# Performance work log

Hardware: AMD Instinct MI355X
Metric: run time of the kernel (lower is better)

## Reference

```python
import jax, jax.numpy as jnp
import numpy as np

B, C, H, W = 4, 3, 128, 128
HID = 128          # hidden_features
L = 6              # hidden_layers
NP = 5             # n_params
DT = 0.1
EPS = 1e-5         # PyG InstanceNorm eps
D_EMB = 1 + 2 + NP             # u + pos(2) + params
D_MSG = 2 * HID + 1 + 2 + NP   # x_i,x_j,u_i-u_j,pos_i-pos_j,vars_i
D_UPD = HID + HID + NP         # x, message, vars


def _build_edges(b, h, w):
    # 8-neighbor grid graph (radius_graph with r=sqrt(2), loop=False),
    # node index = ix*h + iy (x-major, matching create_graph's meshgrid flatten)
    ix, iy = np.meshgrid(np.arange(w), np.arange(h), indexing='ij')
    node = ix * h + iy
    srcs, tgts = [], []
    for dx in (-1, 0, 1):
        for dy in (-1, 0, 1):
            if dx == 0 and dy == 0:
                continue
            t = node[max(0, -dx):w - max(0, dx), max(0, -dy):h - max(0, dy)]
            s = node[max(0, dx):w - max(0, -dx), max(0, dy):h - max(0, -dy)]
            srcs.append(s.ravel()); tgts.append(t.ravel())
    src = np.concatenate(srcs); tgt = np.concatenate(tgts)
    offs = (np.arange(b) * h * w)[:, None]
    src = (src[None, :] + offs).ravel()
    tgt = (tgt[None, :] + offs).ravel()
    return np.stack([src, tgt]).astype(np.int32)


def _lin(key, fan_in, fan_out):
    kw, kb = jax.random.split(key)
    s = 1.0 / np.sqrt(fan_in)
    return (jax.random.uniform(kw, (fan_in, fan_out), jnp.float32, -s, s),
            jax.random.uniform(kb, (fan_out,), jnp.float32, -s, s))


def setup_inputs() -> dict:
    key = jax.random.key(0)
    ks = jax.random.split(key, 32)
    inputs = jax.random.normal(ks[0], (B, C, H, W), jnp.float32)
    case_params = jax.random.uniform(ks[1], (B, NP), jnp.float32, 0.5, 1.5)
    edge_index = jnp.asarray(_build_edges(B, H, W))

    emb_W1, emb_b1 = _lin(ks[2], D_EMB, HID)
    emb_W2, emb_b2 = _lin(ks[3], HID, HID)

    def stack(kbase, fan_in, fan_out):
        Ws, bs = [], []
        for l in range(L):
            Wl, bl = _lin(jax.random.fold_in(kbase, l), fan_in, fan_out)
            Ws.append(Wl); bs.append(bl)
        return jnp.stack(Ws), jnp.stack(bs)

    msg1_W, msg1_b = stack(ks[4], D_MSG, HID)
    msg2_W, msg2_b = stack(ks[5], HID, HID)
    upd1_W, upd1_b = stack(ks[6], D_UPD, HID)
    upd2_W, upd2_b = stack(ks[7], HID, HID)
    out_W1, out_b1 = _lin(ks[8], HID, HID // 2)
    out_W2, out_b2 = _lin(ks[9], HID // 2, 1)

    return dict(inputs=inputs, case_params=case_params, edge_index=edge_index,
                emb_W1=emb_W1, emb_b1=emb_b1, emb_W2=emb_W2, emb_b2=emb_b2,
                msg1_W=msg1_W, msg1_b=msg1_b, msg2_W=msg2_W, msg2_b=msg2_b,
                upd1_W=upd1_W, upd1_b=upd1_b, upd2_W=upd2_W, upd2_b=upd2_b,
                out_W1=out_W1, out_b1=out_b1, out_W2=out_W2, out_b2=out_b2)


def reference(inputs, case_params, edge_index,
              emb_W1, emb_b1, emb_W2, emb_b2,
              msg1_W, msg1_b, msg2_W, msg2_b,
              upd1_W, upd1_b, upd2_W, upd2_b,
              out_W1, out_b1, out_W2, out_b2):
    b, c, h, w = inputs.shape
    n = b * h * w
    swish = lambda x: x * jax.nn.sigmoid(x)

    # graph node features: [b,c,h,w] -> [b*h*w, c]; u = channel 0
    x_nodes = inputs.transpose(0, 2, 3, 1).reshape(-1, c)
    u = x_nodes[:, :1]
    # pos, faithful to create_graph: per-graph meshgrid over (x:w, y:h), x-major flatten
    gx = jnp.linspace(0., 1., w)[:, None] * jnp.ones((h,), inputs.dtype)   # [w,h]
    gy = jnp.ones((w,), inputs.dtype)[:, None] * jnp.linspace(0., 1., h)  # [w,h]
    pos = jnp.stack([gx[None] * case_params[:, 1, None, None],
                     gy[None] * case_params[:, 0, None, None]], axis=-1).reshape(-1, 2)
    params = jnp.repeat(case_params, h * w, axis=0)  # [n, NP]

    src, tgt = edge_index[0], edge_index[1]
    deg = jax.ops.segment_sum(jnp.ones_like(src, dtype=inputs.dtype), tgt,
                              num_segments=n)
    deg = jnp.maximum(deg, 1.)[:, None]

    # embedding MLP
    f = swish(jnp.concatenate([u, pos, params], -1) @ emb_W1 + emb_b1)
    f = swish(f @ emb_W2 + emb_b2)

    for l in range(msg1_W.shape[0]):
        # message: gather -> MLP (formula 8)
        m = jnp.concatenate([f[tgt], f[src], u[tgt] - u[src],
                             pos[tgt] - pos[src], params[tgt]], -1)  # [E, D_MSG]
        m = swish(m @ msg1_W[l] + msg1_b[l])
        m = swish(m @ msg2_W[l] + msg2_b[l])
        # mean-aggregate at target nodes
        agg = jax.ops.segment_sum(m, tgt, num_segments=n) / deg
        # update MLP (formula 9) + residual (in_features == out_features)
        upd = swish(jnp.concatenate([f, agg, params], -1) @ upd1_W[l] + upd1_b[l])
        upd = swish(upd @ upd2_W[l] + upd2_b[l])
        f = f + upd
        # InstanceNorm per graph (affine=False, biased var)
        fg = f.reshape(b, h * w, -1)
        mean = fg.mean(1, keepdims=True)
        var = ((fg - mean) ** 2).mean(1, keepdims=True)
        f = ((fg - mean) * jax.lax.rsqrt(var + EPS)).reshape(n, -1)

    diff = swish(f @ out_W1 + out_b1) @ out_W2 + out_b2  # [n,1]
    out = u + DT * diff
    return out.reshape(b, h, w, 1).transpose(0, 3, 1, 2)  # preds [b,1,h,w]
```

## Files before the change

### kernel.cpp

```cpp
#include <hip/hip_runtime.h>
#include <hip/hip_bf16.h>
#include <math.h>

#define NNODE 65536
#define NBAT  16384
#define NP    5
#define DT    0.1f
#define EPS   1e-5f

typedef __attribute__((ext_vector_type(8))) short short8;
typedef __attribute__((ext_vector_type(4))) float floatx4;

union S8U { short8 s; unsigned int u[4]; };

__device__ __forceinline__ float swishf(float x) {
    return x * __builtin_amdgcn_rcpf(1.f + __expf(-x));
}
__device__ __forceinline__ float asf(unsigned int u) {
    union { unsigned int u; float f; } x; x.u = u; return x.f;
}
__device__ __forceinline__ unsigned short f2b(float f) {
    union { float f; unsigned int u; } x; x.f = f;
    unsigned int r = x.u + 0x7fff + ((x.u >> 16) & 1);
    return (unsigned short)(r >> 16);
}
__device__ __forceinline__ unsigned int pk2(float a, float b) {
    __hip_bfloat162 h = __float22bfloat162_rn(make_float2(a, b));
    union { __hip_bfloat162 h; unsigned int u; } x; x.h = h; return x.u;
}

#define CHP(w, g, r15) ((((w) * 272) + (g) * 17 + (r15)) * 8)

__global__ __launch_bounds__(256) void prep_all(
    const float* __restrict__ msg1_W, const float* __restrict__ msg2_W,
    const float* __restrict__ upd1_W, const float* __restrict__ upd2_W,
    const float* __restrict__ emb_W2, const float* __restrict__ out_W1,
    unsigned short* __restrict__ wPT, unsigned short* __restrict__ wQT,
    unsigned short* __restrict__ w2F, unsigned short* __restrict__ u1aF,
    unsigned short* __restrict__ u1bF, unsigned short* __restrict__ u2F,
    unsigned short* __restrict__ eW2F, unsigned short* __restrict__ O1F)
{
    int blk = blockIdx.x;
    const float* src; unsigned short* dst;
    int ldn = 128, koff, NT = 8, lstride, perm = 1, i0;
    if (blk < 384)       { src = msg1_W; dst = wPT;  koff = 0;   lstride = 264 * 128; i0 = blk; }
    else if (blk < 768)  { src = msg1_W; dst = wQT;  koff = 128; lstride = 264 * 128; i0 = blk - 384; }
    else if (blk < 1152) { src = msg2_W; dst = w2F;  koff = 0;   lstride = 128 * 128; i0 = blk - 768; }
    else if (blk < 1536) { src = upd1_W; dst = u1aF; koff = 0;   lstride = 261 * 128; i0 = blk - 1152; }
    else if (blk < 1920) { src = upd1_W; dst = u1bF; koff = 128; lstride = 261 * 128; i0 = blk - 1536; }
    else if (blk < 2304) { src = upd2_W; dst = u2F;  koff = 0;   lstride = 128 * 128; i0 = blk - 1920; }
    else if (blk < 2368) { src = emb_W2; dst = eW2F; koff = 0;   lstride = 0; perm = 0; i0 = blk - 2304; }
    else                 { src = out_W1; dst = O1F;  koff = 0;   lstride = 0; ldn = 64; NT = 4; i0 = blk - 2368; }
    int i = i0 * 256 + threadIdx.x;
    int nper = NT << 11;
    int l = i / nper;
    int r0 = i - l * nper;
    int t = r0 >> 11;
    int ks = (r0 >> 9) & 3;
    int lane = (r0 >> 3) & 63;
    int j = r0 & 7;
    int lm = lane & 15, lq = lane >> 4;
    int p = ks * 32 + lq * 8 + j;
    int k = perm ? ((p & 7) * 16 + (p >> 3)) : p;
    int n = t * 16 + lm;
    dst[i] = f2b(src[(size_t)l * lstride + (size_t)(koff + k) * ldn + n]);
}

__device__ __forceinline__ void build_normf_frags(
    const float* __restrict__ f, const float* __restrict__ mr,
    int block0, int b, int w, int lm, int lq, short8* afr)
{
    int row = block0 + w * 16 + lm;
#pragma unroll
    for (int ks = 0; ks < 4; ks++) {
        int po = ks * 32 + lq * 8;
        float4 v0 = *(const float4*)(f + (size_t)row * 128 + po);
        float4 v1 = *(const float4*)(f + (size_t)row * 128 + po + 4);
        float4 m0 = *(const float4*)(mr + b * 256 + po);
        float4 m1 = *(const float4*)(mr + b * 256 + po + 4);
        float4 s0 = *(const float4*)(mr + b * 256 + 128 + po);
        float4 s1 = *(const float4*)(mr + b * 256 + 128 + po + 4);
        S8U o;
        o.u[0] = pk2((v0.x - m0.x) * s0.x, (v0.y - m0.y) * s0.y);
        o.u[1] = pk2((v0.z - m0.z) * s0.z, (v0.w - m0.w) * s0.w);
        o.u[2] = pk2((v1.x - m1.x) * s1.x, (v1.y - m1.y) * s1.y);
        o.u[3] = pk2((v1.z - m1.z) * s1.z, (v1.w - m1.w) * s1.w);
        afr[ks] = o.s;
    }
}

__global__ __launch_bounds__(256) void embed_mfma(
    const float* __restrict__ inp, const float* __restrict__ cp,
    const float* __restrict__ W1, const float* __restrict__ b1,
    const unsigned short* __restrict__ W2F, const float* __restrict__ b2,
    float* __restrict__ f, float* __restrict__ u,
    float* __restrict__ posx, float* __restrict__ posy, float* __restrict__ mr)
{
    __shared__ unsigned short lA[4 * 272 * 8];
    __shared__ unsigned short lB[1024 * 8];
    int tid = threadIdx.x;
    int block0 = blockIdx.x * 64;
    if (blockIdx.x < 4) mr[blockIdx.x * 256 + tid] = ((tid >> 7) & 1) ? 1.f : 0.f;
    {
        int r = tid >> 2, p4 = tid & 3;
        int n = block0 + r;
        int b = n >> 14;
        int rr = n & 16383;
        int aa = rr >> 7, cc = rr & 127;
        float uu = inp[b * 3 * NBAT + rr];
        float pxx = (aa * (1.f / 127.f)) * cp[b * NP + 1];
        float pyy = (cc * (1.f / 127.f)) * cp[b * NP + 0];
        if (p4 == 0) { u[n] = uu; posx[n] = pxx; posy[n] = pyy; }
        float e8[8];
        e8[0] = uu; e8[1] = pxx; e8[2] = pyy;
#pragma unroll
        for (int p = 0; p < 5; p++) e8[3 + p] = cp[b * NP + p];
        float a32[32];
        const float4* b4 = (const float4*)(b1 + p4 * 32);
#pragma unroll
        for (int q = 0; q < 8; q++) {
            float4 bv = b4[q];
            a32[q * 4 + 0] = bv.x; a32[q * 4 + 1] = bv.y;
            a32[q * 4 + 2] = bv.z; a32[q * 4 + 3] = bv.w;
        }
#pragma unroll
        for (int i = 0; i < 8; i++) {
            const float4* w4 = (const float4*)(W1 + i * 128 + p4 * 32);
            float ev = e8[i];
#pragma unroll
            for (int q = 0; q < 8; q++) {
                float4 wv = w4[q];
                a32[q * 4 + 0] += ev * wv.x; a32[q * 4 + 1] += ev * wv.y;
                a32[q * 4 + 2] += ev * wv.z; a32[q * 4 + 3] += ev * wv.w;
            }
        }
#pragma unroll
        for (int j = 0; j < 4; j++) {
            S8U o;
#pragma unroll
            for (int q = 0; q < 4; q++)
                o.u[q] = pk2(swishf(a32[j * 8 + 2 * q]), swishf(a32[j * 8 + 2 * q + 1]));
            *(short8*)(lA + CHP(r >> 4, p4 * 4 + j, r & 15)) = o.s;
        }
    }
    int w = tid >> 6, lane = tid & 63, lm = lane & 15, lq = lane >> 4;
    float bias2[8];
#pragma unroll
    for (int t = 0; t < 8; t++) bias2[t] = b2[t * 16 + lm];
    floatx4 acc[8];
#pragma unroll
    for (int t = 0; t < 8; t++) acc[t] = (floatx4)(bias2[t]);
    for (int th = 0; th < 2; th++) {
        if (th) __syncthreads();
#pragma unroll
        for (int i = 0; i < 4; i++)
            *(short8*)(lB + (tid + i * 256) * 8) =
                *(const short8*)(W2F + (th * 1024 + tid + i * 256) * 8);
        __syncthreads();
#pragma unroll
        for (int ks = 0; ks < 4; ks++) {
            short8 a = *(const short8*)(lA + CHP(w, ks * 4 + lq, lm));
#pragma unroll
            for (int t2 = 0; t2 < 4; t2++) {
                short8 bf = *(const short8*)(lB + ((t2 * 4 + ks) * 64 + lane) * 8);
                acc[th * 4 + t2] = __builtin_amdgcn_mfma_f32_16x16x32_bf16(a, bf, acc[th * 4 + t2], 0, 0, 0);
            }
        }
    }
#pragma unroll
    for (int r = 0; r < 4; r++) {
        int nd = block0 + w * 16 + lq * 4 + r;
        float4 v0, v1;
        v0.x = swishf(acc[0][r]); v0.y = swishf(acc[1][r]);
        v0.z = swishf(acc[2][r]); v0.w = swishf(acc[3][r]);
        v1.x = swishf(acc[4][r]); v1.y = swishf(acc[5][r]);
        v1.z = swishf(acc[6][r]); v1.w = swishf(acc[7][r]);
        *(float4*)(f + (size_t)nd * 128 + lm * 8) = v0;
        *(float4*)(f + (size_t)nd * 128 + lm * 8 + 4) = v1;
    }
}

__global__ __launch_bounds__(256) void pqu_kernel(
    const float* __restrict__ f, const float* __restrict__ mr,
    const unsigned short* __restrict__ wPT, const unsigned short* __restrict__ wQT,
    const float* __restrict__ mW, const float* __restrict__ mb,
    const float* __restrict__ u, const float* __restrict__ px,
    const float* __restrict__ py, const float* __restrict__ cp,
    unsigned short* __restrict__ Pn, unsigned short* __restrict__ Qn)
{
    __shared__ unsigned short lB[2048 * 8];
    int tid = threadIdx.x;
    int block0 = blockIdx.x * 64;
    int b = block0 >> 14;
    int w = tid >> 6, lane = tid & 63, lm = lane & 15, lq = lane >> 4;

    short8 afr[4];
    build_normf_frags(f, mr, block0, b, w, lm, lq, afr);

    float u4[4], px4[4], py4[4];
#pragma unroll
    for (int r = 0; r < 4; r++) {
        int nd = block0 + w * 16 + lq * 4 + r;
        u4[r] = u[nd]; px4[r] = px[nd]; py4[r] = py[nd];
    }
    float cp5[5];
#pragma unroll
    for (int p = 0; p < 5; p++) cp5[p] = cp[b * NP + p];
    float wu[8], wx[8], wy[8], pt[8];
#pragma unroll
    for (int t = 0; t < 8; t++) {
        int c = t * 16 + lm;
        wu[t] = mW[256 * 128 + c]; wx[t] = mW[257 * 128 + c]; wy[t] = mW[258 * 128 + c];
        float p0 = mb[c];
#pragma unroll
        for (int p = 0; p < 5; p++) p0 += cp5[p] * mW[(259 + p) * 128 + c];
        pt[t] = p0;
    }

    for (int ph = 0; ph < 2; ph++) {
        const unsigned short* bsrc = (ph == 0) ? wPT : wQT;
        if (ph) __syncthreads();
#pragma unroll
        for (int i = 0; i < 8; i++)
            *(short8*)(lB + (tid + i * 256) * 8) = *(const short8*)(bsrc + (tid + i * 256) * 8);
        __syncthreads();
        floatx4 acc[8];
#pragma unroll
        for (int t = 0; t < 8; t++) acc[t] = (ph == 0) ? (floatx4)(pt[t]) : (floatx4)(0.f);
#pragma unroll
        for (int ks = 0; ks < 4; ks++) {
#pragma unroll
            for (int t = 0; t < 8; t++) {
                short8 bf = *(const short8*)(lB + ((t * 4 + ks) * 64 + lane) * 8);
                acc[t] = __builtin_amdgcn_mfma_f32_16x16x32_bf16(afr[ks], bf, acc[t], 0, 0, 0);
            }
        }
        if (ph == 0) {
#pragma unroll
            for (int r = 0; r < 4; r++) {
                int nd = block0 + w * 16 + lq * 4 + r;
                float sc0 = u4[r], sc1 = px4[r], sc2 = py4[r];
                float v[8];
#pragma unroll
                for (int t = 0; t < 8; t++)
                    v[t] = acc[t][r] + sc0 * wu[t] + sc1 * wx[t] + sc2 * wy[t];
                S8U o;
#pragma unroll
                for (int q = 0; q < 4; q++) o.u[q] = pk2(v[2 * q], v[2 * q + 1]);
                *(short8*)(Pn + (size_t)nd * 128 + lm * 8) = o.s;
            }
        } else {
#pragma unroll
            for (int r = 0; r < 4; r++) {
                int nd = block0 + w * 16 + lq * 4 + r;
                float sc0 = u4[r], sc1 = px4[r], sc2 = py4[r];
                float v[8];
#pragma unroll
                for (int t = 0; t < 8; t++)
                    v[t] = acc[t][r] - (sc0 * wu[t] + sc1 * wx[t] + sc2 * wy[t]);
                S8U o;
#pragma unroll
                for (int q = 0; q < 4; q++) o.u[q] = pk2(v[2 * q], v[2 * q + 1]);
                *(short8*)(Qn + (size_t)nd * 128 + lm * 8) = o.s;
            }
        }
    }
}

__global__ __launch_bounds__(256) void msg_kernel(
    const unsigned short* __restrict__ Pn, const unsigned short* __restrict__ Qn,
    const unsigned short* __restrict__ w2F, const float* __restrict__ b2,
    unsigned short* __restrict__ aggF)
{
    __shared__ unsigned short lB[1024 * 8];
    __shared__ unsigned short lAgg[8 * 128];
    int tid = threadIdx.x;
    int base = blockIdx.x * 8;
    int b = base >> 14;
    int a = (base >> 7) & 127;
    int c0 = base & 127;
    int w = tid >> 6, lane = tid & 63, lm = lane & 15, lq = lane >> 4;
    bool interior = (a > 0) & (a < 127) & (c0 > 0) & (c0 + 8 < 128);

    short8 afr[4];
    {
        int tl = lm >> 3, e = lm & 7;
        int idx = (e < 4) ? e : e + 1;
        int dx = idx / 3 - 1, dy = idx % 3 - 1;
        int cc = c0 + w * 2 + tl;
        int na = a + dx, nc = cc + dy;
        int t = base + w * 2 + tl;
        int s;
        if (interior) s = (b << 14) + (na << 7) + nc;
        else {
            bool valid = (na >= 0) & (na < 128) & (nc >= 0) & (nc < 128);
            s = valid ? ((b << 14) + (na << 7) + nc) : t;
        }
#pragma unroll
        for (int ks = 0; ks < 4; ks++) {
            int po = ks * 32 + lq * 8;
            S8U pv, qv, o;
            pv.s = *(const short8*)(Pn + (size_t)t * 128 + po);
            qv.s = *(const short8*)(Qn + (size_t)s * 128 + po);
#pragma unroll
            for (int q = 0; q < 4; q++) {
                float pl = asf(pv.u[q] << 16), ph = asf(pv.u[q] & 0xffff0000u);
                float ql = asf(qv.u[q] << 16), qh = asf(qv.u[q] & 0xffff0000u);
                o.u[q] = pk2(swishf(pl + ql), swishf(ph + qh));
            }
            afr[ks] = o.s;
        }
    }

    float b2v[8];
#pragma unroll
    for (int t = 0; t < 8; t++) b2v[t] = b2[t * 16 + lm];
    floatx4 acc[8];
#pragma unroll
    for (int t = 0; t < 8; t++) acc[t] = (floatx4)(b2v[t]);
    for (int th = 0; th < 2; th++) {
        if (th) __syncthreads();
#pragma unroll
        for (int i = 0; i < 4; i++)
            *(short8*)(lB + (tid + i * 256) * 8) =
                *(const short8*)(w2F + (th * 1024 + tid + i * 256) * 8);
        __syncthreads();
#pragma unroll
        for (int ks = 0; ks < 4; ks++) {
#pragma unroll
            for (int t2 = 0; t2 < 4; t2++) {
                short8 bf = *(const short8*)(lB + ((t2 * 4 + ks) * 64 + lane) * 8);
                acc[th * 4 + t2] = __builtin_amdgcn_mfma_f32_16x16x32_bf16(afr[ks], bf, acc[th * 4 + t2], 0, 0, 0);
            }
        }
    }

    if (interior) {
        float ov[8];
#pragma unroll
        for (int t = 0; t < 8; t++) {
            float s01 = swishf(acc[t][0]) + swishf(acc[t][1])
                      + swishf(acc[t][2]) + swishf(acc[t][3]);
            ov[t] = s01 + __shfl_xor(s01, 16);
        }
        if ((lq & 1) == 0) {
            int tl = w * 2 + (lq >> 1);
            S8U o;
#pragma unroll
            for (int q = 0; q < 4; q++)
                o.u[q] = pk2(ov[2 * q] * 0.125f, ov[2 * q + 1] * 0.125f);
            *(short8*)(lAgg + tl * 128 + lm * 8) = o.s;
        }
    } else {
        bool vr[4];
#pragma unroll
        for (int r = 0; r < 4; r++) {
            int row16 = lq * 4 + r;
            int tl2 = row16 >> 3, e = row16 & 7;
            int idx = (e < 4) ? e : e + 1;
            int dx = idx / 3 - 1, dy = idx % 3 - 1;
            int cc = c0 + w * 2 + tl2;
            int na = a + dx, nc = cc + dy;
            vr[r] = (na >= 0) & (na < 128) & (nc >= 0) & (nc < 128);
        }
        float ov[8];
#pragma unroll
        for (int t = 0; t < 8; t++) {
            float s01 = 0.f;
#pragma unroll
            for (int r = 0; r < 4; r++)
                s01 += vr[r] ? swishf(acc[t][r]) : 0.f;
            ov[t] = s01 + __shfl_xor(s01, 16);
        }
        if ((lq & 1) == 0) {
            int tl = w * 2 + (lq >> 1);
            int cc = c0 + tl;
            int deg = (1 + (a > 0) + (a < 127)) * (1 + (cc > 0) + (cc < 127)) - 1;
            float inv = 1.f / (float)deg;
            S8U o;
#pragma unroll
            for (int q = 0; q < 4; q++) o.u[q] = pk2(ov[2 * q] * inv, ov[2 * q + 1] * inv);
            *(short8*)(lAgg + tl * 128 + lm * 8) = o.s;
        }
    }
    __syncthreads();
    if (tid < 128) {
        int row8 = tid >> 4, g = tid & 15;
        int n = base + row8;
        size_t lin = (size_t)(n >> 6) * 1024 + (size_t)(((n & 63) >> 4) * 256 + g * 16 + (n & 15));
        *(short8*)(aggF + lin * 8) = *(const short8*)(lAgg + row8 * 128 + g * 8);
    }
}

__global__ __launch_bounds__(256) void updf_kernel(
    float* __restrict__ f, const float* __restrict__ mr,
    const unsigned short* __restrict__ aggF,
    const unsigned short* __restrict__ u1aF, const unsigned short* __restrict__ u1bF,
    const unsigned short* __restrict__ u2F,
    const float* __restrict__ U1, const float* __restrict__ c1,
    const float* __restrict__ c2, const float* __restrict__ cp,
    float* __restrict__ partials)
{
    __shared__ unsigned short lA[4 * 272 * 8];
    __shared__ unsigned short lB[1024 * 8];
    int tid = threadIdx.x;
    int block0 = blockIdx.x * 64;
    int b = block0 >> 14;
    int w = tid >> 6, lane = tid & 63, lm = lane & 15, lq = lane >> 4;

    float cp5[5];
#pragma unroll
    for (int p = 0; p < 5; p++) cp5[p] = cp[b * NP + p];
    float pt[8];
#pragma unroll
    for (int t = 0; t < 8; t++) {
        int c = t * 16 + lm;
        float p0 = c1[c];
#pragma unroll
        for (int p = 0; p < 5; p++) p0 += cp5[p] * U1[(256 + p) * 128 + c];
        pt[t] = p0;
    }

    short8 afr[4];
    build_normf_frags(f, mr, block0, b, w, lm, lq, afr);
    floatx4 acc[8];
#pragma unroll
    for (int t = 0; t < 8; t++) acc[t] = (floatx4)(pt[t]);

    for (int ph = 0; ph < 2; ph++) {
        const unsigned short* bsrc = ph ? u1bF : u1aF;
        if (ph) {
#pragma unroll
            for (int ks = 0; ks < 4; ks++)
                afr[ks] = *(const short8*)(aggF +
                    ((size_t)blockIdx.x * 1024 + w * 256 + (ks * 4 + lq) * 16 + lm) * 8);
        }
        for (int th = 0; th < 2; th++) {
            if (ph | th) __syncthreads();
#pragma unroll
            for (int i = 0; i < 4; i++)
                *(short8*)(lB + (tid + i * 256) * 8) =
                    *(const short8*)(bsrc + (th * 1024 + tid + i * 256) * 8);
            __syncthreads();
#pragma unroll
            for (int ks = 0; ks < 4; ks++) {
#pragma unroll
                for (int t2 = 0; t2 < 4; t2++) {
                    short8 bf = *(const short8*)(lB + ((t2 * 4 + ks) * 64 + lane) * 8);
                    acc[th * 4 + t2] = __builtin_amdgcn_mfma_f32_16x16x32_bf16(afr[ks], bf, acc[th * 4 + t2], 0, 0, 0);
                }
            }
        }
    }

#pragma unroll
    for (int r = 0; r < 4; r++) {
        S8U o;
#pragma unroll
        for (int q = 0; q < 4; q++)
            o.u[q] = pk2(swishf(acc[2 * q][r]), swishf(acc[2 * q + 1][r]));
        *(short8*)(lA + CHP(w, lm, lq * 4 + r)) = o.s;
    }

    float c2v[8];
#pragma unroll
    for (int t = 0; t < 8; t++) c2v[t] = c2[t * 16 + lm];
#pragma unroll
    for (int t = 0; t < 8; t++) acc[t] = (floatx4)(c2v[t]);
    for (int th = 0; th < 2; th++) {
        __syncthreads();
#pragma unroll
        for (int i = 0; i < 4; i++)
            *(short8*)(lB + (tid + i * 256) * 8) =
                *(const short8*)(u2F + (th * 1024 + tid + i * 256) * 8);
        __syncthreads();
#pragma unroll
        for (int ks = 0; ks < 4; ks++) {
            short8 a = *(const short8*)(lA + CHP(w, ks * 4 + lq, lm));
#pragma unroll
            for (int t2 = 0; t2 < 4; t2++) {
                short8 bf = *(const short8*)(lB + ((t2 * 4 + ks) * 64 + lane) * 8);
                acc[th * 4 + t2] = __builtin_amdgcn_mfma_f32_16x16x32_bf16(a, bf, acc[th * 4 + t2], 0, 0, 0);
            }
        }
    }

    float4 me0 = *(const float4*)(mr + b * 256 + lm * 8);
    float4 me1 = *(const float4*)(mr + b * 256 + lm * 8 + 4);
    float4 rs0 = *(const float4*)(mr + b * 256 + 128 + lm * 8);
    float4 rs1 = *(const float4*)(mr + b * 256 + 128 + lm * 8 + 4);
    float ssum[8], ssq[8];
#pragma unroll
    for (int t = 0; t < 8; t++) { ssum[t] = 0.f; ssq[t] = 0.f; }
#pragma unroll
    for (int r = 0; r < 4; r++) {
        int nd = block0 + w * 16 + lq * 4 + r;
        float4 f0 = *(const float4*)(f + (size_t)nd * 128 + lm * 8);
        float4 f1 = *(const float4*)(f + (size_t)nd * 128 + lm * 8 + 4);
        float fn[8];
        fn[0] = (f0.x - me0.x) * rs0.x + swishf(acc[0][r]);
        fn[1] = (f0.y - me0.y) * rs0.y + swishf(acc[1][r]);
        fn[2] = (f0.z - me0.z) * rs0.z + swishf(acc[2][r]);
        fn[3] = (f0.w - me0.w) * rs0.w + swishf(acc[3][r]);
        fn[4] = (f1.x - me1.x) * rs1.x + swishf(acc[4][r]);
        fn[5] = (f1.y - me1.y) * rs1.y + swishf(acc[5][r]);
        fn[6] = (f1.z - me1.z) * rs1.z + swishf(acc[6][r]);
        fn[7] = (f1.w - me1.w) * rs1.w + swishf(acc[7][r]);
        *(float4*)(f + (size_t)nd * 128 + lm * 8) = make_float4(fn[0], fn[1], fn[2], fn[3]);
        *(float4*)(f + (size_t)nd * 128 + lm * 8 + 4) = make_float4(fn[4], fn[5], fn[6], fn[7]);
#pragma unroll
        for (int t = 0; t < 8; t++) { ssum[t] += fn[t]; ssq[t] += fn[t] * fn[t]; }
    }
#pragma unroll
    for (int t = 0; t < 8; t++) {
        ssum[t] += __shfl_xor(ssum[t], 16); ssum[t] += __shfl_xor(ssum[t], 32);
        ssq[t]  += __shfl_xor(ssq[t], 16);  ssq[t]  += __shfl_xor(ssq[t], 32);
    }
    __syncthreads();
    float* red = (float*)lA;
    if (lq == 0) {
#pragma unroll
        for (int t = 0; t < 8; t++) {
            red[w * 256 + lm * 8 + t] = ssum[t];
            red[w * 256 + 128 + lm * 8 + t] = ssq[t];
        }
    }
    __syncthreads();
    {
        float v = red[tid] + red[256 + tid] + red[512 + tid] + red[768 + tid];
        partials[(size_t)blockIdx.x * 256 + tid] = v;
    }
}

__global__ __launch_bounds__(256) void finalize_kernel(
    const float* __restrict__ partials, float* __restrict__ mr)
{
    __shared__ float s[256];
    int b = blockIdx.x, tid = threadIdx.x;
    float acc = 0.f;
    const float* p = partials + (size_t)b * 256 * 256 + tid;
#pragma unroll 8
    for (int i = 0; i < 256; i++) acc += p[i * 256];
    s[tid] = acc;
    __syncthreads();
    if (tid < 128) {
        float mean = s[tid] * (1.f / 16384.f);
        float var = s[128 + tid] * (1.f / 16384.f) - mean * mean;
        mr[b * 256 + tid] = mean;
        mr[b * 256 + 128 + tid] = rsqrtf(var + EPS);
    }
}

__global__ __launch_bounds__(256) void out_head(
    const float* __restrict__ f, const float* __restrict__ mr,
    const unsigned short* __restrict__ O1F, const float* __restrict__ ob1,
    const float* __restrict__ O2, const float* __restrict__ ob2,
    const float* __restrict__ u, float* __restrict__ out)
{
    __shared__ unsigned short lB[1024 * 8];
    int tid = threadIdx.x;
    int block0 = blockIdx.x * 64;
    int b = block0 >> 14;
    int w = tid >> 6, lane = tid & 63, lm = lane & 15, lq = lane >> 4;
#pragma unroll
    for (int i = 0; i < 4; i++)
        *(short8*)(lB + (tid + i * 256) * 8) = *(const short8*)(O1F + (tid + i * 256) * 8);
    short8 afr[4];
    build_normf_frags(f, mr, block0, b, w, lm, lq, afr);
    float b1v[4], o2v[4];
#pragma unroll
    for (int t = 0; t < 4; t++) {
        b1v[t] = ob1[t * 16 + lm];
        o2v[t] = O2[t * 16 + lm];
    }
    __syncthreads();
    floatx4 acc[4];
#pragma unroll
    for (int t = 0; t < 4; t++) acc[t] = (floatx4)(b1v[t]);
#pragma unroll
    for (int ks = 0; ks < 4; ks++) {
#pragma unroll
        for (int t = 0; t < 4; t++) {
            short8 bf = *(const short8*)(lB + ((t * 4 + ks) * 64 + lane) * 8);
            acc[t] = __builtin_amdgcn_mfma_f32_16x16x32_bf16(afr[ks], bf, acc[t], 0, 0, 0);
        }
    }
    float ob2v = ob2[0];
#pragma unroll
    for (int r = 0; r < 4; r++) {
        float s = 0.f;
#pragma unroll
        for (int t = 0; t < 4; t++) s += swishf(acc[t][r]) * o2v[t];
        s += __shfl_xor(s, 1); s += __shfl_xor(s, 2);
        s += __shfl_xor(s, 4); s += __shfl_xor(s, 8);
        if (lm == 0) {
            int nd = block0 + w * 16 + lq * 4 + r;
            out[nd] = u[nd] + DT * (s + ob2v);
        }
    }
}

extern "C" void kernel_launch(void* const* d_in, const int* in_sizes, int n_in,
                              void* d_out, int out_size, void* d_ws, size_t ws_size,
                              hipStream_t stream)
{
    const float* inputs = (const float*)d_in[0];
    const float* cp     = (const float*)d_in[1];
    const float* emb_W1 = (const float*)d_in[3];
    const float* emb_b1 = (const float*)d_in[4];
    const float* emb_W2 = (const float*)d_in[5];
    const float* emb_b2 = (const float*)d_in[6];
    const float* msg1_W = (const float*)d_in[7];
    const float* msg1_b = (const float*)d_in[8];
    const float* msg2_W = (const float*)d_in[9];
    const float* msg2_b = (const float*)d_in[10];
    const float* upd1_W = (const float*)d_in[11];
    const float* upd1_b = (const float*)d_in[12];
    const float* upd2_W = (const float*)d_in[13];
    const float* upd2_b = (const float*)d_in[14];
    const float* out_W1 = (const float*)d_in[15];
    const float* out_b1 = (const float*)d_in[16];
    const float* out_W2 = (const float*)d_in[17];
    const float* out_b2 = (const float*)d_in[18];
    float* out = (float*)d_out;

    char* base = (char*)d_ws;
    size_t off = 0;
    float* f     = (float*)(base + off); off += (size_t)NNODE * 128 * 4;
    unsigned short* Pn   = (unsigned short*)(base + off); off += (size_t)NNODE * 128 * 2;
    unsigned short* Qn   = (unsigned short*)(base + off); off += (size_t)NNODE * 128 * 2;
    unsigned short* aggF = (unsigned short*)(base + off); off += (size_t)NNODE * 128 * 2;
    float* u    = (float*)(base + off); off += NNODE * 4;
    float* posx = (float*)(base + off); off += NNODE * 4;
    float* posy = (float*)(base + off); off += NNODE * 4;
    float* partials = (float*)(base + off); off += 1024 * 256 * 4;
    float* mrbuf = (float*)(base + off); off += 1024 * 4;
    unsigned short* wPT  = (unsigned short*)(base + off); off += 6 * 16384 * 2;
    unsigned short* wQT  = (unsigned short*)(base + off); off += 6 * 16384 * 2;
    unsigned short* w2F  = (unsigned short*)(base + off); off += 6 * 16384 * 2;
    unsigned short* u1aF = (unsigned short*)(base + off); off += 6 * 16384 * 2;
    unsigned short* u1bF = (unsigned short*)(base + off); off += 6 * 16384 * 2;
    unsigned short* u2F  = (unsigned short*)(base + off); off += 6 * 16384 * 2;
    unsigned short* eW2F = (unsigned short*)(base + off); off += 16384 * 2;
    unsigned short* O1F  = (unsigned short*)(base + off); off += 8192 * 2;

    prep_all<<<2400, 256, 0, stream>>>(msg1_W, msg2_W, upd1_W, upd2_W, emb_W2, out_W1,
                                       wPT, wQT, w2F, u1aF, u1bF, u2F, eW2F, O1F);
    embed_mfma<<<1024, 256, 0, stream>>>(inputs, cp, emb_W1, emb_b1, eW2F, emb_b2,
                                         f, u, posx, posy, mrbuf);
    for (int l = 0; l < 6; l++) {
        pqu_kernel<<<1024, 256, 0, stream>>>(f, mrbuf,
            wPT + (size_t)l * 16384, wQT + (size_t)l * 16384,
            msg1_W + (size_t)l * 264 * 128, msg1_b + (size_t)l * 128,
            u, posx, posy, cp, Pn, Qn);
        msg_kernel<<<8192, 256, 0, stream>>>(Pn, Qn,
            w2F + (size_t)l * 16384, msg2_b + (size_t)l * 128, aggF);
        updf_kernel<<<1024, 256, 0, stream>>>(f, mrbuf, aggF,
            u1aF + (size_t)l * 16384, u1bF + (size_t)l * 16384, u2F + (size_t)l * 16384,
            upd1_W + (size_t)l * 261 * 128, upd1_b + (size_t)l * 128,
            upd2_b + (size_t)l * 128, cp, partials);
        finalize_kernel<<<4, 256, 0, stream>>>(partials, mrbuf);
    }
    out_head<<<1024, 256, 0, stream>>>(f, mrbuf, O1F, out_b1, out_W2, out_b2, u, out);
}
```

Baseline: 752.6 us.

## Store node features in bf16 and fuse InstanceNorm finalize into update kernel

```diff
diff --git a/kernel.cpp b/kernel.cpp
--- a/kernel.cpp
+++ b/kernel.cpp
@@ -67,24 +67,27 @@
 }
 
 __device__ __forceinline__ void build_normf_frags(
-    const float* __restrict__ f, const float* __restrict__ mr,
+    const unsigned short* __restrict__ fB, const float* __restrict__ mr,
     int block0, int b, int w, int lm, int lq, short8* afr)
 {
     int row = block0 + w * 16 + lm;
 #pragma unroll
     for (int ks = 0; ks < 4; ks++) {
         int po = ks * 32 + lq * 8;
-        float4 v0 = *(const float4*)(f + (size_t)row * 128 + po);
-        float4 v1 = *(const float4*)(f + (size_t)row * 128 + po + 4);
+        S8U v; v.s = *(const short8*)(fB + (size_t)row * 128 + po);
         float4 m0 = *(const float4*)(mr + b * 256 + po);
         float4 m1 = *(const float4*)(mr + b * 256 + po + 4);
         float4 s0 = *(const float4*)(mr + b * 256 + 128 + po);
         float4 s1 = *(const float4*)(mr + b * 256 + 128 + po + 4);
         S8U o;
-        o.u[0] = pk2((v0.x - m0.x) * s0.x, (v0.y - m0.y) * s0.y);
-        o.u[1] = pk2((v0.z - m0.z) * s0.z, (v0.w - m0.w) * s0.w);
-        o.u[2] = pk2((v1.x - m1.x) * s1.x, (v1.y - m1.y) * s1.y);
-        o.u[3] = pk2((v1.z - m1.z) * s1.z, (v1.w - m1.w) * s1.w);
+        o.u[0] = pk2((asf(v.u[0] << 16) - m0.x) * s0.x,
+                     (asf(v.u[0] & 0xffff0000u) - m0.y) * s0.y);
+        o.u[1] = pk2((asf(v.u[1] << 16) - m0.z) * s0.z,
+                     (asf(v.u[1] & 0xffff0000u) - m0.w) * s0.w);
+        o.u[2] = pk2((asf(v.u[2] << 16) - m1.x) * s1.x,
+                     (asf(v.u[2] & 0xffff0000u) - m1.y) * s1.y);
+        o.u[3] = pk2((asf(v.u[3] << 16) - m1.z) * s1.z,
+                     (asf(v.u[3] & 0xffff0000u) - m1.w) * s1.w);
         afr[ks] = o.s;
     }
 }
@@ -93,14 +96,16 @@
     const float* __restrict__ inp, const float* __restrict__ cp,
     const float* __restrict__ W1, const float* __restrict__ b1,
     const unsigned short* __restrict__ W2F, const float* __restrict__ b2,
-    float* __restrict__ f, float* __restrict__ u,
-    float* __restrict__ posx, float* __restrict__ posy, float* __restrict__ mr)
+    unsigned short* __restrict__ fB, float* __restrict__ u,
+    float* __restrict__ posx, float* __restrict__ posy, float* __restrict__ mr,
+    int* __restrict__ cnt)
 {
     __shared__ unsigned short lA[4 * 272 * 8];
     __shared__ unsigned short lB[1024 * 8];
     int tid = threadIdx.x;
     int block0 = blockIdx.x * 64;
     if (blockIdx.x < 4) mr[blockIdx.x * 256 + tid] = ((tid >> 7) & 1) ? 1.f : 0.f;
+    if (blockIdx.x == 4 && tid < 24) cnt[tid] = 0;
     {
         int r = tid >> 2, p4 = tid & 3;
         int n = block0 + r;
@@ -170,18 +175,17 @@
 #pragma unroll
     for (int r = 0; r < 4; r++) {
         int nd = block0 + w * 16 + lq * 4 + r;
-        float4 v0, v1;
-        v0.x = swishf(acc[0][r]); v0.y = swishf(acc[1][r]);
-        v0.z = swishf(acc[2][r]); v0.w = swishf(acc[3][r]);
-        v1.x = swishf(acc[4][r]); v1.y = swishf(acc[5][r]);
-        v1.z = swishf(acc[6][r]); v1.w = swishf(acc[7][r]);
-        *(float4*)(f + (size_t)nd * 128 + lm * 8) = v0;
-        *(float4*)(f + (size_t)nd * 128 + lm * 8 + 4) = v1;
+        S8U o;
+        o.u[0] = pk2(swishf(acc[0][r]), swishf(acc[1][r]));
+        o.u[1] = pk2(swishf(acc[2][r]), swishf(acc[3][r]));
+        o.u[2] = pk2(swishf(acc[4][r]), swishf(acc[5][r]));
+        o.u[3] = pk2(swishf(acc[6][r]), swishf(acc[7][r]));
+        *(short8*)(fB + (size_t)nd * 128 + lm * 8) = o.s;
     }
 }
 
 __global__ __launch_bounds__(256) void pqu_kernel(
-    const float* __restrict__ f, const float* __restrict__ mr,
+    const unsigned short* __restrict__ fB, const float* __restrict__ mr,
     const unsigned short* __restrict__ wPT, const unsigned short* __restrict__ wQT,
     const float* __restrict__ mW, const float* __restrict__ mb,
     const float* __restrict__ u, const float* __restrict__ px,
@@ -195,7 +199,7 @@
     int w = tid >> 6, lane = tid & 63, lm = lane & 15, lq = lane >> 4;
 
     short8 afr[4];
-    build_normf_frags(f, mr, block0, b, w, lm, lq, afr);
+    build_normf_frags(fB, mr, block0, b, w, lm, lq, afr);
 
     float u4[4], px4[4], py4[4];
 #pragma unroll
@@ -393,180 +397,182 @@
 }
 
 __global__ __launch_bounds__(256) void updf_kernel(
-    float* __restrict__ f, const float* __restrict__ mr,
+    unsigned short* __restrict__ fB, float* __restrict__ mr,
     const unsigned short* __restrict__ aggF,
     const unsigned short* __restrict__ u1aF, const unsigned short* __restrict__ u1bF,
     const unsigned short* __restrict__ u2F,
     const float* __restrict__ U1, const float* __restrict__ c1,
     const float* __restrict__ c2, const float* __restrict__ cp,
-    float* __restrict__ partials)
+    float* __restrict__ partials, int* __restrict__ cnt)
 {
     __shared__ unsigned short lA[4 * 272 * 8];
+    __shared__ unsigned short lB[1024 * 8];
+    __shared__ bool isLast;
+    int tid = threadIdx.x;
+    int block0 = blockIdx.x * 64;
+    int b = block0 >> 14;
+    int w = tid >> 6, lane = tid & 63, lm = lane & 15, lq = lane >> 4;
+
+    float cp5[5];
+#pragma unroll
+    for (int p = 0; p < 5; p++) cp5[p] = cp[b * NP + p];
+    float pt[8];
+#pragma unroll
+    for (int t = 0; t < 8; t++) {
+        int c = t * 16 + lm;
+        float p0 = c1[c];
+#pragma unroll
+        for (int p = 0; p < 5; p++) p0 += cp5[p] * U1[(256 + p) * 128 + c];
+        pt[t] = p0;
+    }
+
+    short8 afr[4];
+    build_normf_frags(fB, mr, block0, b, w, lm, lq, afr);
+    floatx4 acc[8];
+#pragma unroll
+    for (int t = 0; t < 8; t++) acc[t] = (floatx4)(pt[t]);
+
+    for (int ph = 0; ph < 2; ph++) {
+        const unsigned short* bsrc = ph ? u1bF : u1aF;
+        if (ph) {
+#pragma unroll
+            for (int ks = 0; ks < 4; ks++)
+                afr[ks] = *(const short8*)(aggF +
+                    ((size_t)blockIdx.x * 1024 + w * 256 + (ks * 4 + lq) * 16 + lm) * 8);
+        }
+        for (int th = 0; th < 2; th++) {
+            if (ph | th) __syncthreads();
+#pragma unroll
+            for (int i = 0; i < 4; i++)
+                *(short8*)(lB + (tid + i * 256) * 8) =
+                    *(const short8*)(bsrc + (th * 1024 + tid + i * 256) * 8);
+            __syncthreads();
+#pragma unroll
+            for (int ks = 0; ks < 4; ks++) {
+#pragma unroll
+                for (int t2 = 0; t2 < 4; t2++) {
+                    short8 bf = *(const short8*)(lB + ((t2 * 4 + ks) * 64 + lane) * 8);
+                    acc[th * 4 + t2] = __builtin_amdgcn_mfma_f32_16x16x32_bf16(afr[ks], bf, acc[th * 4 + t2], 0, 0, 0);
+                }
+            }
+        }
+    }
+
+#pragma unroll
+    for (int r = 0; r < 4; r++) {
+        S8U o;
+#pragma unroll
+        for (int q = 0; q < 4; q++)
+            o.u[q] = pk2(swishf(acc[2 * q][r]), swishf(acc[2 * q + 1][r]));
+        *(short8*)(lA + CHP(w, lm, lq * 4 + r)) = o.s;
+    }
+
+    float c2v[8];
+#pragma unroll
+    for (int t = 0; t < 8; t++) c2v[t] = c2[t * 16 + lm];
+#pragma unroll
+    for (int t = 0; t < 8; t++) acc[t] = (floatx4)(c2v[t]);
+    for (int th = 0; th < 2; th++) {
+        __syncthreads();
+#pragma unroll
+        for (int i = 0; i < 4; i++)
+            *(short8*)(lB + (tid + i * 256) * 8) =
+                *(const short8*)(u2F + (th * 1024 + tid + i * 256) * 8);
+        __syncthreads();
+#pragma unroll
+        for (int ks = 0; ks < 4; ks++) {
+            short8 a = *(const short8*)(lA + CHP(w, ks * 4 + lq, lm));
+#pragma unroll
+            for (int t2 = 0; t2 < 4; t2++) {
+                short8 bf = *(const short8*)(lB + ((t2 * 4 + ks) * 64 + lane) * 8);
+                acc[th * 4 + t2] = __builtin_amdgcn_mfma_f32_16x16x32_bf16(a, bf, acc[th * 4 + t2], 0, 0, 0);
+            }
+        }
+    }
+
+    float4 me0 = *(const float4*)(mr + b * 256 + lm * 8);
+    float4 me1 = *(const float4*)(mr + b * 256 + lm * 8 + 4);
+    float4 rs0 = *(const float4*)(mr + b * 256 + 128 + lm * 8);
+    float4 rs1 = *(const float4*)(mr + b * 256 + 128 + lm * 8 + 4);
+    float ssum[8], ssq[8];
+#pragma unroll
+    for (int t = 0; t < 8; t++) { ssum[t] = 0.f; ssq[t] = 0.f; }
+#pragma unroll
+    for (int r = 0; r < 4; r++) {
+        int nd = block0 + w * 16 + lq * 4 + r;
+        S8U fo; fo.s = *(const short8*)(fB + (size_t)nd * 128 + lm * 8);
+        float fn[8];
+        fn[0] = (asf(fo.u[0] << 16)        - me0.x) * rs0.x + swishf(acc[0][r]);
+        fn[1] = (asf(fo.u[0] & 0xffff0000u) - me0.y) * rs0.y + swishf(acc[1][r]);
+        fn[2] = (asf(fo.u[1] << 16)        - me0.z) * rs0.z + swishf(acc[2][r]);
+        fn[3] = (asf(fo.u[1] & 0xffff0000u) - me0.w) * rs0.w + swishf(acc[3][r]);
+        fn[4] = (asf(fo.u[2] << 16)        - me1.x) * rs1.x + swishf(acc[4][r]);
+        fn[5] = (asf(fo.u[2] & 0xffff0000u) - me1.y) * rs1.y + swishf(acc[5][r]);
+        fn[6] = (asf(fo.u[3] << 16)        - me1.z) * rs1.z + swishf(acc[6][r]);
+        fn[7] = (asf(fo.u[3] & 0xffff0000u) - me1.w) * rs1.w + swishf(acc[7][r]);
+        S8U o;
+        o.u[0] = pk2(fn[0], fn[1]); o.u[1] = pk2(fn[2], fn[3]);
+        o.u[2] = pk2(fn[4], fn[5]); o.u[3] = pk2(fn[6], fn[7]);
+        *(short8*)(fB + (size_t)nd * 128 + lm * 8) = o.s;
+#pragma unroll
+        for (int t = 0; t < 8; t++) { ssum[t] += fn[t]; ssq[t] += fn[t] * fn[t]; }
+    }
+#pragma unroll
+    for (int t = 0; t < 8; t++) {
+        ssum[t] += __shfl_xor(ssum[t], 16); ssum[t] += __shfl_xor(ssum[t], 32);
+        ssq[t]  += __shfl_xor(ssq[t], 16);  ssq[t]  += __shfl_xor(ssq[t], 32);
+    }
+    __syncthreads();
+    float* red = (float*)lA;
+    if (lq == 0) {
+#pragma unroll
+        for (int t = 0; t < 8; t++) {
+            red[w * 256 + lm * 8 + t] = ssum[t];
+            red[w * 256 + 128 + lm * 8 + t] = ssq[t];
+        }
+    }
+    __syncthreads();
+    {
+        float v = red[tid] + red[256 + tid] + red[512 + tid] + red[768 + tid];
+        partials[(size_t)blockIdx.x * 256 + tid] = v;
+    }
+    __threadfence();
+    __syncthreads();
+    if (tid == 0) isLast = (atomicAdd(&cnt[b], 1) == 255);
+    __syncthreads();
+    if (isLast) {
+        __threadfence();
+        float acc2 = 0.f;
+        const float* pp = partials + (size_t)b * 65536 + tid;
+#pragma unroll 8
+        for (int i = 0; i < 256; i++) acc2 += pp[i * 256];
+        red[tid] = acc2;
+        __syncthreads();
+        if (tid < 128) {
+            float mean = red[tid] * (1.f / 16384.f);
+            float var = red[128 + tid] * (1.f / 16384.f) - mean * mean;
+            mr[b * 256 + tid] = mean;
+            mr[b * 256 + 128 + tid] = rsqrtf(var + EPS);
+        }
+    }
+}
+
+__global__ __launch_bounds__(256) void out_head(
+    const unsigned short* __restrict__ fB, const float* __restrict__ mr,
+    const unsigned short* __restrict__ O1F, const float* __restrict__ ob1,
+    const float* __restrict__ O2, const float* __restrict__ ob2,
+    const float* __restrict__ u, float* __restrict__ out)
+{
     __shared__ unsigned short lB[1024 * 8];
     int tid = threadIdx.x;
     int block0 = blockIdx.x * 64;
     int b = block0 >> 14;
     int w = tid >> 6, lane = tid & 63, lm = lane & 15, lq = lane >> 4;
-
-    float cp5[5];
-#pragma unroll
-    for (int p = 0; p < 5; p++) cp5[p] = cp[b * NP + p];
-    float pt[8];
-#pragma unroll
-    for (int t = 0; t < 8; t++) {
-        int c = t * 16 + lm;
-        float p0 = c1[c];
-#pragma unroll
-        for (int p = 0; p < 5; p++) p0 += cp5[p] * U1[(256 + p) * 128 + c];
-        pt[t] = p0;
-    }
-
-    short8 afr[4];
-    build_normf_frags(f, mr, block0, b, w, lm, lq, afr);
-    floatx4 acc[8];
-#pragma unroll
-    for (int t = 0; t < 8; t++) acc[t] = (floatx4)(pt[t]);
-
-    for (int ph = 0; ph < 2; ph++) {
-        const unsigned short* bsrc = ph ? u1bF : u1aF;
-        if (ph) {
-#pragma unroll
-            for (int ks = 0; ks < 4; ks++)
-                afr[ks] = *(const short8*)(aggF +
-                    ((size_t)blockIdx.x * 1024 + w * 256 + (ks * 4 + lq) * 16 + lm) * 8);
-        }
-        for (int th = 0; th < 2; th++) {
-            if (ph | th) __syncthreads();
-#pragma unroll
-            for (int i = 0; i < 4; i++)
-                *(short8*)(lB + (tid + i * 256) * 8) =
-                    *(const short8*)(bsrc + (th * 1024 + tid + i * 256) * 8);
-            __syncthreads();
-#pragma unroll
-            for (int ks = 0; ks < 4; ks++) {
-#pragma unroll
-                for (int t2 = 0; t2 < 4; t2++) {
-                    short8 bf = *(const short8*)(lB + ((t2 * 4 + ks) * 64 + lane) * 8);
-                    acc[th * 4 + t2] = __builtin_amdgcn_mfma_f32_16x16x32_bf16(afr[ks], bf, acc[th * 4 + t2], 0, 0, 0);
-                }
-            }
-        }
-    }
-
-#pragma unroll
-    for (int r = 0; r < 4; r++) {
-        S8U o;
-#pragma unroll
-        for (int q = 0; q < 4; q++)
-            o.u[q] = pk2(swishf(acc[2 * q][r]), swishf(acc[2 * q + 1][r]));
-        *(short8*)(lA + CHP(w, lm, lq * 4 + r)) = o.s;
-    }
-
-    float c2v[8];
-#pragma unroll
-    for (int t = 0; t < 8; t++) c2v[t] = c2[t * 16 + lm];
-#pragma unroll
-    for (int t = 0; t < 8; t++) acc[t] = (floatx4)(c2v[t]);
-    for (int th = 0; th < 2; th++) {
-        __syncthreads();
-#pragma unroll
-        for (int i = 0; i < 4; i++)
-            *(short8*)(lB + (tid + i * 256) * 8) =
-                *(const short8*)(u2F + (th * 1024 + tid + i * 256) * 8);
-        __syncthreads();
-#pragma unroll
-        for (int ks = 0; ks < 4; ks++) {
-            short8 a = *(const short8*)(lA + CHP(w, ks * 4 + lq, lm));
-#pragma unroll
-            for (int t2 = 0; t2 < 4; t2++) {
-                short8 bf = *(const short8*)(lB + ((t2 * 4 + ks) * 64 + lane) * 8);
-                acc[th * 4 + t2] = __builtin_amdgcn_mfma_f32_16x16x32_bf16(a, bf, acc[th * 4 + t2], 0, 0, 0);
-            }
-        }
-    }
-
-    float4 me0 = *(const float4*)(mr + b * 256 + lm * 8);
-    float4 me1 = *(const float4*)(mr + b * 256 + lm * 8 + 4);
-    float4 rs0 = *(const float4*)(mr + b * 256 + 128 + lm * 8);
-    float4 rs1 = *(const float4*)(mr + b * 256 + 128 + lm * 8 + 4);
-    float ssum[8], ssq[8];
-#pragma unroll
-    for (int t = 0; t < 8; t++) { ssum[t] = 0.f; ssq[t] = 0.f; }
-#pragma unroll
-    for (int r = 0; r < 4; r++) {
-        int nd = block0 + w * 16 + lq * 4 + r;
-        float4 f0 = *(const float4*)(f + (size_t)nd * 128 + lm * 8);
-        float4 f1 = *(const float4*)(f + (size_t)nd * 128 + lm * 8 + 4);
-        float fn[8];
-        fn[0] = (f0.x - me0.x) * rs0.x + swishf(acc[0][r]);
-        fn[1] = (f0.y - me0.y) * rs0.y + swishf(acc[1][r]);
-        fn[2] = (f0.z - me0.z) * rs0.z + swishf(acc[2][r]);
-        fn[3] = (f0.w - me0.w) * rs0.w + swishf(acc[3][r]);
-        fn[4] = (f1.x - me1.x) * rs1.x + swishf(acc[4][r]);
-        fn[5] = (f1.y - me1.y) * rs1.y + swishf(acc[5][r]);
-        fn[6] = (f1.z - me1.z) * rs1.z + swishf(acc[6][r]);
-        fn[7] = (f1.w - me1.w) * rs1.w + swishf(acc[7][r]);
-        *(float4*)(f + (size_t)nd * 128 + lm * 8) = make_float4(fn[0], fn[1], fn[2], fn[3]);
-        *(float4*)(f + (size_t)nd * 128 + lm * 8 + 4) = make_float4(fn[4], fn[5], fn[6], fn[7]);
-#pragma unroll
-        for (int t = 0; t < 8; t++) { ssum[t] += fn[t]; ssq[t] += fn[t] * fn[t]; }
-    }
-#pragma unroll
-    for (int t = 0; t < 8; t++) {
-        ssum[t] += __shfl_xor(ssum[t], 16); ssum[t] += __shfl_xor(ssum[t], 32);
-        ssq[t]  += __shfl_xor(ssq[t], 16);  ssq[t]  += __shfl_xor(ssq[t], 32);
-    }
-    __syncthreads();
-    float* red = (float*)lA;
-    if (lq == 0) {
-#pragma unroll
-        for (int t = 0; t < 8; t++) {
-            red[w * 256 + lm * 8 + t] = ssum[t];
-            red[w * 256 + 128 + lm * 8 + t] = ssq[t];
-        }
-    }
-    __syncthreads();
-    {
-        float v = red[tid] + red[256 + tid] + red[512 + tid] + red[768 + tid];
-        partials[(size_t)blockIdx.x * 256 + tid] = v;
-    }
-}
-
-__global__ __launch_bounds__(256) void finalize_kernel(
-    const float* __restrict__ partials, float* __restrict__ mr)
-{
-    __shared__ float s[256];
-    int b = blockIdx.x, tid = threadIdx.x;
-    float acc = 0.f;
-    const float* p = partials + (size_t)b * 256 * 256 + tid;
-#pragma unroll 8
-    for (int i = 0; i < 256; i++) acc += p[i * 256];
-    s[tid] = acc;
-    __syncthreads();
-    if (tid < 128) {
-        float mean = s[tid] * (1.f / 16384.f);
-        float var = s[128 + tid] * (1.f / 16384.f) - mean * mean;
-        mr[b * 256 + tid] = mean;
-        mr[b * 256 + 128 + tid] = rsqrtf(var + EPS);
-    }
-}
-
-__global__ __launch_bounds__(256) void out_head(
-    const float* __restrict__ f, const float* __restrict__ mr,
-    const unsigned short* __restrict__ O1F, const float* __restrict__ ob1,
-    const float* __restrict__ O2, const float* __restrict__ ob2,
-    const float* __restrict__ u, float* __restrict__ out)
-{
-    __shared__ unsigned short lB[1024 * 8];
-    int tid = threadIdx.x;
-    int block0 = blockIdx.x * 64;
-    int b = block0 >> 14;
-    int w = tid >> 6, lane = tid & 63, lm = lane & 15, lq = lane >> 4;
 #pragma unroll
     for (int i = 0; i < 4; i++)
         *(short8*)(lB + (tid + i * 256) * 8) = *(const short8*)(O1F + (tid + i * 256) * 8);
     short8 afr[4];
-    build_normf_frags(f, mr, block0, b, w, lm, lq, afr);
+    build_normf_frags(fB, mr, block0, b, w, lm, lq, afr);
     float b1v[4], o2v[4];
 #pragma unroll
     for (int t = 0; t < 4; t++) {
@@ -626,7 +632,7 @@
 
     char* base = (char*)d_ws;
     size_t off = 0;
-    float* f     = (float*)(base + off); off += (size_t)NNODE * 128 * 4;
+    unsigned short* fB   = (unsigned short*)(base + off); off += (size_t)NNODE * 128 * 2;
     unsigned short* Pn   = (unsigned short*)(base + off); off += (size_t)NNODE * 128 * 2;
     unsigned short* Qn   = (unsigned short*)(base + off); off += (size_t)NNODE * 128 * 2;
     unsigned short* aggF = (unsigned short*)(base + off); off += (size_t)NNODE * 128 * 2;
@@ -635,6 +641,7 @@
     float* posy = (float*)(base + off); off += NNODE * 4;
     float* partials = (float*)(base + off); off += 1024 * 256 * 4;
     float* mrbuf = (float*)(base + off); off += 1024 * 4;
+    int* cnt = (int*)(base + off); off += 64 * 4;
     unsigned short* wPT  = (unsigned short*)(base + off); off += 6 * 16384 * 2;
     unsigned short* wQT  = (unsigned short*)(base + off); off += 6 * 16384 * 2;
     unsigned short* w2F  = (unsigned short*)(base + off); off += 6 * 16384 * 2;
@@ -647,19 +654,18 @@
     prep_all<<<2400, 256, 0, stream>>>(msg1_W, msg2_W, upd1_W, upd2_W, emb_W2, out_W1,
                                        wPT, wQT, w2F, u1aF, u1bF, u2F, eW2F, O1F);
     embed_mfma<<<1024, 256, 0, stream>>>(inputs, cp, emb_W1, emb_b1, eW2F, emb_b2,
-                                         f, u, posx, posy, mrbuf);
+                                         fB, u, posx, posy, mrbuf, cnt);
     for (int l = 0; l < 6; l++) {
-        pqu_kernel<<<1024, 256, 0, stream>>>(f, mrbuf,
+        pqu_kernel<<<1024, 256, 0, stream>>>(fB, mrbuf,
             wPT + (size_t)l * 16384, wQT + (size_t)l * 16384,
             msg1_W + (size_t)l * 264 * 128, msg1_b + (size_t)l * 128,
             u, posx, posy, cp, Pn, Qn);
         msg_kernel<<<8192, 256, 0, stream>>>(Pn, Qn,
             w2F + (size_t)l * 16384, msg2_b + (size_t)l * 128, aggF);
-        updf_kernel<<<1024, 256, 0, stream>>>(f, mrbuf, aggF,
+        updf_kernel<<<1024, 256, 0, stream>>>(fB, mrbuf, aggF,
             u1aF + (size_t)l * 16384, u1bF + (size_t)l * 16384, u2F + (size_t)l * 16384,
             upd1_W + (size_t)l * 261 * 128, upd1_b + (size_t)l * 128,
-            upd2_b + (size_t)l * 128, cp, partials);
-        finalize_kernel<<<4, 256, 0, stream>>>(partials, mrbuf);
-    }
-    out_head<<<1024, 256, 0, stream>>>(f, mrbuf, O1F, out_b1, out_W2, out_b2, u, out);
-}
+            upd2_b + (size_t)l * 128, cp, partials, cnt + l * 4);
+    }
+    out_head<<<1024, 256, 0, stream>>>(fB, mrbuf, O1F, out_b1, out_W2, out_b2, u, out);
+}
```

Measured after the change: 1.295 ms. +72.1%, slower.
